# Kernel tuning notes

Hardware: AMD Instinct MI355X
Metric: run time of the kernel (lower is better)

The kernel has to match this reference:

```python
import jax, jax.numpy as jnp
import numpy as np

# Nemotron-H Mamba2 mixer decoder layer (prefill path, zero initial states,
# full context lengths). Dims per init_kwargs.
B, S, H = 1, 256, 4096
NH, P, G, N, K = 128, 64, 8, 128, 4   # num_heads, head_dim, n_groups, ssm_state_size, conv_kernel
D_INNER = NH * P                      # 8192
D_STATE = G * N                       # 1024
CONV_DIM = D_INNER + 2 * D_STATE      # 10240
IN_OUT = D_INNER + CONV_DIM + NH      # 18560
EPS = 1e-6


def setup_inputs() -> dict:
    key = jax.random.key(0)
    ks = jax.random.split(key, 8)
    sc = 0.02
    return {
        "hidden_states": jax.random.normal(ks[0], (B, S, H), jnp.float32),
        "conv_state": jnp.zeros((B, CONV_DIM, K - 1), jnp.float32),
        "ssm_state": jnp.zeros((B, NH, P, N), jnp.float32),
        "norm_weight": jnp.ones((H,), jnp.float32),
        "w_in": jax.random.normal(ks[1], (IN_OUT, H), jnp.float32) * sc,
        "conv_w": jax.random.normal(ks[2], (CONV_DIM, K), jnp.float32) * 0.2,
        "conv_b": jnp.zeros((CONV_DIM,), jnp.float32),
        "A_log": jax.random.uniform(ks[3], (NH,), jnp.float32, 0.0, 1.0),
        "D_param": jax.random.normal(ks[4], (NH,), jnp.float32) * 0.1,
        "dt_bias": jax.random.normal(ks[5], (NH,), jnp.float32) * 0.1,
        "ssm_norm_weight": jnp.ones((D_INNER,), jnp.float32),
        "w_out": jax.random.normal(ks[6], (H, D_INNER), jnp.float32) * sc,
    }


def _rmsnorm(x, w, eps=EPS):
    var = jnp.mean(x * x, axis=-1, keepdims=True)
    return x * jax.lax.rsqrt(var + eps) * w


def reference(hidden_states, conv_state, ssm_state, norm_weight, w_in, conv_w,
              conv_b, A_log, D_param, dt_bias, ssm_norm_weight, w_out):
    resid = hidden_states
    h = _rmsnorm(hidden_states, norm_weight)           # pre-mixer RMSNorm
    proj = jnp.einsum('bsh,oh->bso', h, w_in)          # in_proj [B,S,18560]
    gate = proj[..., :D_INNER]
    xconv = proj[..., D_INNER:D_INNER + CONV_DIM]
    dt = proj[..., D_INNER + CONV_DIM:]                # [B,S,NH]

    # depthwise causal conv1d, initial left context = conv_state
    xc = jnp.swapaxes(xconv, 1, 2)                     # [B,CONV_DIM,S]
    xpad = jnp.concatenate([conv_state, xc], axis=-1)  # [B,CONV_DIM,S+K-1]
    conv_state_out = xpad[:, :, -(K - 1):]
    y = conv_b[None, :, None]
    for j in range(K):                                 # K=4 taps, unrolled
        y = y + conv_w[:, j][None, :, None] * xpad[:, :, j:j + S]
    y = jax.nn.silu(jnp.swapaxes(y, 1, 2))             # [B,S,CONV_DIM]

    xs = y[..., :D_INNER].reshape(B, S, NH, P)
    Bs = y[..., D_INNER:D_INNER + D_STATE].reshape(B, S, G, N)
    Cs = y[..., D_INNER + D_STATE:].reshape(B, S, G, N)

    A = -jnp.exp(A_log)                                # [NH]
    dtp = jax.nn.softplus(dt + dt_bias)                # [B,S,NH]
    rep = NH // G
    Bh = jnp.repeat(Bs, rep, axis=2)                   # [B,S,NH,N]
    Ch = jnp.repeat(Cs, rep, axis=2)

    def step(state, inp):
        x_t, b_t, c_t, dt_t = inp                      # [B,NH,P],[B,NH,N],[B,NH,N],[B,NH]
        dA = jnp.exp(dt_t * A)                         # [B,NH]
        state = state * dA[..., None, None] + (dt_t[..., None] * x_t)[..., None] * b_t[:, :, None, :]
        y_t = jnp.einsum('bhpn,bhn->bhp', state, c_t)
        return state, y_t

    inps = (jnp.swapaxes(xs, 0, 1), jnp.swapaxes(Bh, 0, 1),
            jnp.swapaxes(Ch, 0, 1), jnp.swapaxes(dtp, 0, 1))
    ssm_state_out, ys = jax.lax.scan(step, ssm_state, inps)
    ys = jnp.swapaxes(ys, 0, 1) + D_param[None, None, :, None] * xs
    ssm_out = ys.reshape(B, S, D_INNER)

    # gated grouped RMSNorm (group_size = D_INNER // G = 1024)
    gated = ssm_out * jax.nn.silu(gate)
    gsize = D_INNER // G
    gg = gated.reshape(B, S, D_INNER // gsize, gsize)
    var = jnp.mean(gg * gg, axis=-1, keepdims=True)
    normed = (gg * jax.lax.rsqrt(var + EPS)).reshape(B, S, D_INNER) * ssm_norm_weight

    out = jnp.einsum('bsd,hd->bsh', normed, w_out)     # out_proj
    return resid + out, conv_state_out, ssm_state_out
```

## Files before the change

kernel.cpp:

```cpp
#include <hip/hip_runtime.h>
#include <hip/hip_bf16.h>

#define Sq 256
#define Hd 4096
#define NH 128
#define Pd 64
#define Gg 8
#define Nn 128
#define D_INNER 8192
#define D_STATE 1024
#define CONV_DIM 10240
#define IN_OUT 18560
#define DT_COL0 18432
#define EPSI 1e-6f

typedef _Float16 f16x8 __attribute__((ext_vector_type(8)));
typedef _Float16 f16x2 __attribute__((ext_vector_type(2)));
typedef float f32x4 __attribute__((ext_vector_type(4)));

__device__ inline ushort f2h(float f) {
  _Float16 h = (_Float16)f;
  return __builtin_bit_cast(ushort, h);
}
__device__ inline float h2f(ushort u) {
  return (float)__builtin_bit_cast(_Float16, u);
}
__device__ inline ushort f2h_lo(float f, ushort hi) {
  float hf = (float)__builtin_bit_cast(_Float16, hi);
  _Float16 l = (_Float16)(f - hf);
  return __builtin_bit_cast(ushort, l);
}
__device__ inline f16x2 pkrtz(float a, float b) {
  return __builtin_bit_cast(f16x2, __builtin_amdgcn_cvt_pkrtz(a, b));
}

__global__ __launch_bounds__(256) void rmsnorm_k(const float* __restrict__ x,
                                                 const float* __restrict__ w,
                                                 ushort* __restrict__ h_hi,
                                                 ushort* __restrict__ h_lo) {
  int s = blockIdx.x, t = threadIdx.x;
  const float4* row = reinterpret_cast<const float4*>(x + (size_t)s * Hd);
  const float4* wv  = reinterpret_cast<const float4*>(w);
  float4 v[4];
  float ss = 0.f;
#pragma unroll
  for (int i = 0; i < 4; i++) {
    v[i] = row[t + i * 256];
    ss += v[i].x * v[i].x + v[i].y * v[i].y + v[i].z * v[i].z + v[i].w * v[i].w;
  }
#pragma unroll
  for (int off = 32; off > 0; off >>= 1) ss += __shfl_xor(ss, off);
  __shared__ float red[4];
  if ((t & 63) == 0) red[t >> 6] = ss;
  __syncthreads();
  ss = red[0] + red[1] + red[2] + red[3];
  float scale = rsqrtf(ss * (1.f / (float)Hd) + EPSI);
  ushort4* hh = reinterpret_cast<ushort4*>(h_hi + (size_t)s * Hd);
  ushort4* hl = reinterpret_cast<ushort4*>(h_lo + (size_t)s * Hd);
#pragma unroll
  for (int i = 0; i < 4; i++) {
    float4 wi = wv[t + i * 256];
    float f0 = v[i].x * scale * wi.x, f1 = v[i].y * scale * wi.y;
    float f2 = v[i].z * scale * wi.z, f3 = v[i].w * scale * wi.w;
    ushort4 oh, ol;
    oh.x = f2h(f0); ol.x = f2h_lo(f0, oh.x);
    oh.y = f2h(f1); ol.y = f2h_lo(f1, oh.y);
    oh.z = f2h(f2); ol.z = f2h_lo(f2, oh.z);
    oh.w = f2h(f3); ol.w = f2h_lo(f3, oh.w);
    hh[t + i * 256] = oh;
    hl[t + i * 256] = ol;
  }
}

__global__ __launch_bounds__(256) void gemm_t128(const ushort* __restrict__ A,
                                                 const float* __restrict__ B,
                                                 float* __restrict__ C0,
                                                 ushort* __restrict__ Cp,
                                                 int ldc, int K, int kLen) {
  __shared__ __align__(16) ushort As[2][128 * 32];
  __shared__ __align__(16) ushort Bs[2][128 * 32];
  int t = threadIdx.x;
  int wave = t >> 6, lane = t & 63;
  int wr = wave >> 1, wc = wave & 1;
  int frow = lane & 15, gq = lane >> 4;
  int coltile = blockIdx.x >> 1;
  int rowBase = (blockIdx.x & 1) * 128;
  int bcol = coltile * 128;
  int z = blockIdx.z;
  int kStart = z * kLen;

  int ar = t >> 2;
  int ax = (ar >> 1) & 3;
  const ushort* ApG0 = A + (size_t)(rowBase + ar) * K + kStart + ((t & 3) ^ ax) * 8;
  const ushort* ApG1 = ApG0 + (size_t)64 * K;
  char* dstA0 = (char*)&As[0][0] + wave * 1024;
  char* dstA1 = (char*)&As[0][0] + 4096 + wave * 1024;

  int brow = t >> 1, bhalf = t & 1;
  int bx = (brow >> 1) & 3;
  const float* BpG = B + (size_t)(bcol + brow) * K + kStart + bhalf * 16;
  int bslot0 = ((2 * bhalf) ^ bx) * 16;
  int bslot1 = ((2 * bhalf + 1) ^ bx) * 16;
  float4 rb[4];

  f32x4 acc[4][4] = {};
  const int NT = kLen / 32;

#define ISSUE_B(kk) { _Pragma("unroll") for (int j = 0; j < 4; ++j) \
                        rb[j] = *(const float4*)(BpG + (kk) + j * 4); }
#define DMA_A(p, kk) { \
    __builtin_amdgcn_global_load_lds( \
        (const __attribute__((address_space(1))) void*)(ApG0 + (kk)), \
        (__attribute__((address_space(3))) void*)(dstA0 + (p) * 8192), 16, 0, 0); \
    __builtin_amdgcn_global_load_lds( \
        (const __attribute__((address_space(1))) void*)(ApG1 + (kk)), \
        (__attribute__((address_space(3))) void*)(dstA1 + (p) * 8192), 16, 0, 0); }
#define WRITE_B(p) { \
    union { f16x2 h2[8]; uint4 q[2]; } u; \
    u.h2[0] = pkrtz(rb[0].x, rb[0].y); u.h2[1] = pkrtz(rb[0].z, rb[0].w); \
    u.h2[2] = pkrtz(rb[1].x, rb[1].y); u.h2[3] = pkrtz(rb[1].z, rb[1].w); \
    u.h2[4] = pkrtz(rb[2].x, rb[2].y); u.h2[5] = pkrtz(rb[2].z, rb[2].w); \
    u.h2[6] = pkrtz(rb[3].x, rb[3].y); u.h2[7] = pkrtz(rb[3].z, rb[3].w); \
    char* bb = (char*)&Bs[0][0] + (p) * 8192 + brow * 64; \
    *(uint4*)(bb + bslot0) = u.q[0]; \
    *(uint4*)(bb + bslot1) = u.q[1]; }

  ISSUE_B(0)
  DMA_A(0, 0)
  WRITE_B(0)
  __syncthreads();

  for (int i = 0; i < NT; ++i) {
    int cur = i & 1;
    if (i + 1 < NT) {
      ISSUE_B((i + 1) * 32)
      DMA_A(cur ^ 1, (i + 1) * 32)
    }
    f16x8 af[4], bf[4];
#pragma unroll
    for (int m = 0; m < 4; ++m) {
      int row = wr * 64 + m * 16 + frow;
      af[m] = *(const f16x8*)((const char*)&As[0][0] + cur * 8192 + row * 64 +
                              ((gq ^ ((row >> 1) & 3)) * 16));
    }
#pragma unroll
    for (int n = 0; n < 4; ++n) {
      int row = wc * 64 + n * 16 + frow;
      bf[n] = *(const f16x8*)((const char*)&Bs[0][0] + cur * 8192 + row * 64 +
                              ((gq ^ ((row >> 1) & 3)) * 16));
    }
#pragma unroll
    for (int m = 0; m < 4; ++m)
#pragma unroll
      for (int n = 0; n < 4; ++n)
        acc[m][n] = __builtin_amdgcn_mfma_f32_16x16x32_f16(af[m], bf[n], acc[m][n], 0, 0, 0);
    __builtin_amdgcn_sched_barrier(0);
    if (i + 1 < NT) WRITE_B(cur ^ 1)
    __syncthreads();
  }
#undef ISSUE_B
#undef DMA_A
#undef WRITE_B

  if (z == 0) {
#pragma unroll
    for (int m = 0; m < 4; ++m) {
      int row0 = rowBase + wr * 64 + m * 16 + (lane >> 4) * 4;
#pragma unroll
      for (int n = 0; n < 4; ++n) {
        int col = bcol + wc * 64 + n * 16 + frow;
#pragma unroll
        for (int r = 0; r < 4; ++r)
          C0[(size_t)(row0 + r) * ldc + col] = acc[m][n][r];
      }
    }
  } else {
    ushort* Cz = Cp + (size_t)(z - 1) * Sq * ldc;
#pragma unroll
    for (int m = 0; m < 4; ++m) {
      int row0 = rowBase + wr * 64 + m * 16 + (lane >> 4) * 4;
#pragma unroll
      for (int n = 0; n < 4; ++n) {
        int col = bcol + wc * 64 + n * 16 + frow;
#pragma unroll
        for (int r = 0; r < 4; ++r)
          Cz[(size_t)(row0 + r) * ldc + col] = f2h(acc[m][n][r]);
      }
    }
  }
}

template<int BN, bool SPLIT>
__global__ __launch_bounds__(256) void gemm_mfma(const ushort* __restrict__ A_hi,
                                                 const ushort* __restrict__ A_lo,
                                                 const float* __restrict__ B,
                                                 float* __restrict__ C,
                                                 int ldc, int K, int kLen,
                                                 int bcol0, int M) {
  constexpr int BK = 64;
  constexpr int LDA = 72;
  constexpr int N_REP = BN / 32;
  constexpr int BQN = (BN == 128) ? 8 : 4;
  __shared__ __align__(16) ushort As[64 * LDA];
  __shared__ __align__(16) ushort Bs[BN * LDA];
  __shared__ __align__(16) ushort AsL[SPLIT ? 64 * LDA : 1];
  __shared__ __align__(16) ushort BsL[SPLIT ? BN * LDA : 1];

  int t = threadIdx.x;
  int wave = t >> 6, lane = t & 63;
  int wr = wave >> 1, wc = wave & 1;
  int frow = lane & 15, fk = (lane >> 4) * 8;
  int rowBase = blockIdx.x * 64;
  int bcol = bcol0 + blockIdx.y * BN;
  int ccol = blockIdx.y * BN;
  int kStart = blockIdx.z * kLen;
  C += (size_t)blockIdx.z * M * ldc;

  int arow = t >> 2, ak = (t & 3) * 16;
  const ushort* Ap  = A_hi + (size_t)(rowBase + arow) * K + ak;
  const ushort* ApL = SPLIT ? (A_lo + (size_t)(rowBase + arow) * K + ak) : nullptr;

  int brow, bq;
  if constexpr (BN == 128) { brow = t >> 1; bq = (t & 1) * 32; }
  else                     { brow = t >> 2; bq = (t & 3) * 16; }
  const float* Bp = B + (size_t)(bcol + brow) * K + bq;

  f32x4 acc[2][N_REP] = {};
  uint4 aPre[2], aPreL[2];
  float4 bPre[BQN];

  auto loadK = [&](int kk) {
    aPre[0] = *reinterpret_cast<const uint4*>(Ap + kk);
    aPre[1] = *reinterpret_cast<const uint4*>(Ap + kk + 8);
    if constexpr (SPLIT) {
      aPreL[0] = *reinterpret_cast<const uint4*>(ApL + kk);
      aPreL[1] = *reinterpret_cast<const uint4*>(ApL + kk + 8);
    }
#pragma unroll
    for (int j = 0; j < BQN; ++j)
      bPre[j] = *reinterpret_cast<const float4*>(Bp + kk + j * 4);
  };

  loadK(kStart);
  for (int ki = 0; ki < kLen; ki += BK) {
    __syncthreads();
    *reinterpret_cast<uint4*>(&As[arow * LDA + ak])     = aPre[0];
    *reinterpret_cast<uint4*>(&As[arow * LDA + ak + 8]) = aPre[1];
    if constexpr (SPLIT) {
      *reinterpret_cast<uint4*>(&AsL[arow * LDA + ak])     = aPreL[0];
      *reinterpret_cast<uint4*>(&AsL[arow * LDA + ak + 8]) = aPreL[1];
    }
    {
      ushort hb[BQN * 4];
      ushort lb[SPLIT ? BQN * 4 : 1];
      const float* bf = reinterpret_cast<const float*>(bPre);
#pragma unroll
      for (int j = 0; j < BQN * 4; ++j) {
        hb[j] = f2h(bf[j]);
        if constexpr (SPLIT) lb[j] = f2h_lo(bf[j], hb[j]);
      }
#pragma unroll
      for (int j = 0; j < BQN / 2; ++j)
        *reinterpret_cast<uint4*>(&Bs[brow * LDA + bq + j * 8]) =
            reinterpret_cast<const uint4*>(hb)[j];
      if constexpr (SPLIT) {
#pragma unroll
        for (int j = 0; j < BQN / 2; ++j)
          *reinterpret_cast<uint4*>(&BsL[brow * LDA + bq + j * 8]) =
              reinterpret_cast<const uint4*>(lb)[j];
      }
    }
    __syncthreads();
    if (ki + BK < kLen) loadK(kStart + ki + BK);
    f16x8 af[2][2], bfv[N_REP][2];
    f16x8 afL[SPLIT ? 2 : 1][2], bfL[SPLIT ? N_REP : 1][2];
#pragma unroll
    for (int m = 0; m < 2; ++m)
#pragma unroll
      for (int kh = 0; kh < 2; ++kh) {
        af[m][kh] = *reinterpret_cast<const f16x8*>(
            &As[(wr * 32 + m * 16 + frow) * LDA + kh * 32 + fk]);
        if constexpr (SPLIT)
          afL[m][kh] = *reinterpret_cast<const f16x8*>(
              &AsL[(wr * 32 + m * 16 + frow) * LDA + kh * 32 + fk]);
      }
#pragma unroll
    for (int n = 0; n < N_REP; ++n)
#pragma unroll
      for (int kh = 0; kh < 2; ++kh) {
        bfv[n][kh] = *reinterpret_cast<const f16x8*>(
            &Bs[(wc * (BN / 2) + n * 16 + frow) * LDA + kh * 32 + fk]);
        if constexpr (SPLIT)
          bfL[n][kh] = *reinterpret_cast<const f16x8*>(
              &BsL[(wc * (BN / 2) + n * 16 + frow) * LDA + kh * 32 + fk]);
      }
#pragma unroll
    for (int kh = 0; kh < 2; ++kh)
#pragma unroll
      for (int m = 0; m < 2; ++m)
#pragma unroll
        for (int n = 0; n < N_REP; ++n) {
          acc[m][n] = __builtin_amdgcn_mfma_f32_16x16x32_f16(af[m][kh], bfv[n][kh], acc[m][n], 0, 0, 0);
          if constexpr (SPLIT) {
            acc[m][n] = __builtin_amdgcn_mfma_f32_16x16x32_f16(af[m][kh], bfL[n][kh], acc[m][n], 0, 0, 0);
            acc[m][n] = __builtin_amdgcn_mfma_f32_16x16x32_f16(afL[m][kh], bfv[n][kh], acc[m][n], 0, 0, 0);
          }
        }
  }

#pragma unroll
  for (int m = 0; m < 2; ++m) {
    int row0 = rowBase + wr * 32 + m * 16 + (lane >> 4) * 4;
#pragma unroll
    for (int n = 0; n < N_REP; ++n) {
      int col = ccol + wc * (BN / 2) + n * 16 + frow;
#pragma unroll
      for (int r = 0; r < 4; ++r)
        C[(size_t)(row0 + r) * ldc + col] = acc[m][n][r];
    }
  }
}

__global__ __launch_bounds__(256) void reduce_in_k(float* __restrict__ proj,
                                                   const ushort* __restrict__ pp) {
  int i = blockIdx.x * 256 + threadIdx.x;
  const size_t PL = (size_t)Sq * IN_OUT;
  float4 o = reinterpret_cast<const float4*>(proj)[i];
#pragma unroll
  for (int zz = 0; zz < 3; ++zz) {
    ushort4 hv = reinterpret_cast<const ushort4*>(pp + zz * PL)[i];
    o.x += h2f(hv.x); o.y += h2f(hv.y); o.z += h2f(hv.z); o.w += h2f(hv.w);
  }
  reinterpret_cast<float4*>(proj)[i] = o;
}

__global__ __launch_bounds__(256) void conv_silu_k(const float* __restrict__ proj,
                                                   const float* __restrict__ cstate,
                                                   const float* __restrict__ cw,
                                                   const float* __restrict__ cb,
                                                   float* __restrict__ y,
                                                   float* __restrict__ out1) {
  int s = blockIdx.y;
  if (s == Sq) {
    int c = blockIdx.x * 256 + threadIdx.x;
#pragma unroll
    for (int tt = 0; tt < 3; ++tt)
      out1[c * 3 + tt] = proj[(size_t)(Sq - 3 + tt) * IN_OUT + D_INNER + c];
    return;
  }
  int c = blockIdx.x * 256 + threadIdx.x;
  float acc = cb[c];
  float4 w4 = *reinterpret_cast<const float4*>(cw + c * 4);
  float wj[4] = {w4.x, w4.y, w4.z, w4.w};
#pragma unroll
  for (int j = 0; j < 4; j++) {
    int si = s + j - 3;
    float v = (si < 0) ? cstate[c * 3 + (si + 3)]
                       : proj[(size_t)si * IN_OUT + D_INNER + c];
    acc += wj[j] * v;
  }
  float sig = 1.f / (1.f + expf(-acc));
  y[(size_t)s * CONV_DIM + c] = acc * sig;
}

#define CS 16
__global__ __launch_bounds__(256) void ssm_scan_k(const float* __restrict__ y_conv,
                                                  const float* __restrict__ dtfix,
                                                  const float* __restrict__ dt_bias,
                                                  const float* __restrict__ sstate_in,
                                                  const float* __restrict__ A_log,
                                                  const float* __restrict__ D_param,
                                                  float* __restrict__ ys_out,
                                                  float* __restrict__ sstate_out) {
  int h = blockIdx.x >> 2;
  int pb = (blockIdx.x & 3) * 16;
  int t = threadIdx.x;
  int ng = t & 15, pl = t >> 4;
  int g = h >> 4;
  float A = -expf(A_log[h]);
  float Dp = D_param[h];
  float bias = dt_bias[h];

  float st[8];
  {
    const float* sp = sstate_in + ((size_t)h * Pd + pb + pl) * Nn + ng * 8;
    float4 v = *reinterpret_cast<const float4*>(sp);
    float4 w = *reinterpret_cast<const float4*>(sp + 4);
    st[0] = v.x; st[1] = v.y; st[2] = v.z; st[3] = v.w;
    st[4] = w.x; st[5] = w.y; st[6] = w.z; st[7] = w.w;
  }

  __shared__ __align__(16) float ybuf[CS][272];
  __shared__ float dts[CS];
  int lr = t >> 4;
  int lc = t & 15;

  for (int ch = 0; ch < Sq / CS; ++ch) {
    int s0 = ch * CS;
    __syncthreads();
    const float* rowp = y_conv + (size_t)(s0 + lr) * CONV_DIM;
#pragma unroll
    for (int j = 0; j < 5; ++j) {
      int c = lc + 16 * j;
      if (c < 68) {
        const float* src;
        int off;
        if (c < 4)       { src = rowp + h * 64 + pb;                      off = c * 4; }
        else if (c < 36) { src = rowp + D_INNER + g * 128;                off = (c - 4) * 4; }
        else             { src = rowp + D_INNER + D_STATE + g * 128;      off = (c - 36) * 4; }
        int dst = (c < 4) ? c * 4 : (c < 36 ? 16 + (c - 4) * 4 : 144 + (c - 36) * 4);
        *reinterpret_cast<float4*>(&ybuf[lr][dst]) = *reinterpret_cast<const float4*>(src + off);
      }
    }
    if (t < CS) {
      float v = bias;
      int idx = (s0 + t) * NH + h;
#pragma unroll
      for (int zz = 0; zz < 32; ++zz) v += dtfix[zz * (Sq * NH) + idx];
      dts[t] = (v > 20.f) ? v : log1pf(expf(v));
    }
    __syncthreads();

#pragma unroll 4
    for (int stp = 0; stp < CS; ++stp) {
      float dt = dts[stp];
      float dA = expf(dt * A);
      float x0 = ybuf[stp][pl];
      float dtx = dt * x0;
      float4 b0 = *reinterpret_cast<const float4*>(&ybuf[stp][16 + ng * 8]);
      float4 b1 = *reinterpret_cast<const float4*>(&ybuf[stp][16 + ng * 8 + 4]);
      float4 c0 = *reinterpret_cast<const float4*>(&ybuf[stp][144 + ng * 8]);
      float4 c1 = *reinterpret_cast<const float4*>(&ybuf[stp][144 + ng * 8 + 4]);
      float y0;
      st[0] = st[0] * dA + dtx * b0.x;  y0  = st[0] * c0.x;
      st[1] = st[1] * dA + dtx * b0.y;  y0 += st[1] * c0.y;
      st[2] = st[2] * dA + dtx * b0.z;  y0 += st[2] * c0.z;
      st[3] = st[3] * dA + dtx * b0.w;  y0 += st[3] * c0.w;
      st[4] = st[4] * dA + dtx * b1.x;  y0 += st[4] * c1.x;
      st[5] = st[5] * dA + dtx * b1.y;  y0 += st[5] * c1.y;
      st[6] = st[6] * dA + dtx * b1.z;  y0 += st[6] * c1.z;
      st[7] = st[7] * dA + dtx * b1.w;  y0 += st[7] * c1.w;
      y0 += __shfl_xor(y0, 1); y0 += __shfl_xor(y0, 2);
      y0 += __shfl_xor(y0, 4); y0 += __shfl_xor(y0, 8);
      if (ng == 0)
        ys_out[(size_t)(s0 + stp) * D_INNER + h * 64 + pb + pl] = y0 + Dp * x0;
    }
  }

  float* so = sstate_out + ((size_t)h * Pd + pb + pl) * Nn + ng * 8;
  *reinterpret_cast<float4*>(so)     = make_float4(st[0], st[1], st[2], st[3]);
  *reinterpret_cast<float4*>(so + 4) = make_float4(st[4], st[5], st[6], st[7]);
}

__global__ __launch_bounds__(256) void gated_norm_k(const float* __restrict__ ys,
                                                    const float* __restrict__ proj,
                                                    const float* __restrict__ w,
                                                    ushort* __restrict__ out_h) {
  int s = blockIdx.x, g = blockIdx.y, t = threadIdx.x;
  float vals[4];
  float ss = 0.f;
#pragma unroll
  for (int i = 0; i < 4; i++) {
    int d = g * 1024 + i * 256 + t;
    float gate = proj[(size_t)s * IN_OUT + d];
    float v = ys[(size_t)s * D_INNER + d] * (gate / (1.f + expf(-gate)));
    vals[i] = v;
    ss += v * v;
  }
#pragma unroll
  for (int off = 32; off > 0; off >>= 1) ss += __shfl_xor(ss, off);
  __shared__ float red[4];
  if ((t & 63) == 0) red[t >> 6] = ss;
  __syncthreads();
  ss = red[0] + red[1] + red[2] + red[3];
  float scale = rsqrtf(ss * (1.f / 1024.f) + EPSI);
#pragma unroll
  for (int i = 0; i < 4; i++) {
    int d = g * 1024 + i * 256 + t;
    out_h[(size_t)s * D_INNER + d] = f2h(vals[i] * scale * w[d]);
  }
}

__global__ __launch_bounds__(256) void reduce_out_k(const float* __restrict__ p0,
                                                    const ushort* __restrict__ pph,
                                                    const float* __restrict__ hidden,
                                                    float* __restrict__ out0) {
  int i = blockIdx.x * 256 + threadIdx.x;
  const size_t PL = (size_t)Sq * Hd;
  float4 o = reinterpret_cast<const float4*>(hidden)[i];
  float4 a = reinterpret_cast<const float4*>(p0)[i];
  o.x += a.x; o.y += a.y; o.z += a.z; o.w += a.w;
#pragma unroll
  for (int zz = 0; zz < 15; ++zz) {
    ushort4 hv = reinterpret_cast<const ushort4*>(pph + zz * PL)[i];
    o.x += h2f(hv.x); o.y += h2f(hv.y); o.z += h2f(hv.z); o.w += h2f(hv.w);
  }
  reinterpret_cast<float4*>(out0)[i] = o;
}

extern "C" void kernel_launch(void* const* d_in, const int* in_sizes, int n_in,
                              void* d_out, int out_size, void* d_ws, size_t ws_size,
                              hipStream_t stream) {
  const float* hidden    = (const float*)d_in[0];
  const float* cstate_in = (const float*)d_in[1];
  const float* sstate_in = (const float*)d_in[2];
  const float* norm_w    = (const float*)d_in[3];
  const float* w_in      = (const float*)d_in[4];
  const float* conv_w    = (const float*)d_in[5];
  const float* conv_b    = (const float*)d_in[6];
  const float* A_log     = (const float*)d_in[7];
  const float* D_param   = (const float*)d_in[8];
  const float* dt_bias   = (const float*)d_in[9];
  const float* ssm_nw    = (const float*)d_in[10];
  const float* w_out     = (const float*)d_in[11];

  float* out0 = (float*)d_out;
  float* out1 = out0 + (size_t)Sq * Hd;
  float* out2 = out1 + (size_t)CONV_DIM * 3;

  ushort* h_hi  = (ushort*)d_ws;
  ushort* h_lo  = h_hi + (size_t)Sq * Hd;
  float*  proj  = (float*)(h_lo + (size_t)Sq * Hd);
  ushort* pp_in = (ushort*)(proj + (size_t)Sq * IN_OUT);
  float*  y_conv = (float*)pp_in;
  float*  dtp   = y_conv + (size_t)Sq * CONV_DIM;
  float*  ys    = dtp + (size_t)Sq * NH;
  ushort* ys_h  = (ushort*)(ys + (size_t)Sq * D_INNER);
  float*  dtfix = (float*)(ys_h + (size_t)Sq * D_INNER);
  float*  op0    = (float*)d_ws;
  ushort* pp_out = (ushort*)(op0 + (size_t)Sq * Hd);

  rmsnorm_k<<<Sq, 256, 0, stream>>>(hidden, norm_w, h_hi, h_lo);
  gemm_t128<<<dim3(2 * (IN_OUT / 128), 1, 4), 256, 0, stream>>>(
      h_hi, w_in, proj, pp_in, IN_OUT, Hd, Hd / 4);
  reduce_in_k<<<(Sq * IN_OUT / 4) / 256, 256, 0, stream>>>(proj, pp_in);
  gemm_mfma<64, true><<<dim3(4, 2, 32), 256, 0, stream>>>(
      h_hi, h_lo, w_in, dtfix, NH, Hd, Hd / 32, DT_COL0, Sq);
  conv_silu_k<<<dim3(CONV_DIM / 256, Sq + 1), 256, 0, stream>>>(
      proj, cstate_in, conv_w, conv_b, y_conv, out1);
  ssm_scan_k<<<NH * 4, 256, 0, stream>>>(y_conv, dtfix, dt_bias, sstate_in,
                                         A_log, D_param, ys, out2);
  gated_norm_k<<<dim3(Sq, Gg), 256, 0, stream>>>(ys, proj, ssm_nw, ys_h);
  gemm_t128<<<dim3(2 * (Hd / 128), 1, 16), 256, 0, stream>>>(
      ys_h, w_out, op0, pp_out, Hd, D_INNER, D_INNER / 16);
  reduce_out_k<<<(Sq * Hd / 4) / 256, 256, 0, stream>>>(op0, pp_out, hidden, out0);
}
```

Before: 349.0 us.

## Widen GEMM tile to full 256 rows with 512-thread blocks sharing B

The GEMM kernel now covers all 256 sequence rows in one block of 8 waves instead of splitting rows across two 128-row blocks. Each block converts and stages the fp32 weight tile to fp16 once rather than twice, which halves global weight reads and conversion work. In exchange the grid has half as many blocks, each block uses more LDS, and fewer blocks fit on a CU, so latency hiding may suffer on the smaller out_proj grid.

```diff
diff --git a/kernel.cpp b/kernel.cpp
--- a/kernel.cpp
+++ b/kernel.cpp
@@ -72,58 +72,51 @@
   }
 }
 
-__global__ __launch_bounds__(256) void gemm_t128(const ushort* __restrict__ A,
+__global__ __launch_bounds__(512) void gemm_w256(const ushort* __restrict__ A,
                                                  const float* __restrict__ B,
                                                  float* __restrict__ C0,
                                                  ushort* __restrict__ Cp,
                                                  int ldc, int K, int kLen) {
-  __shared__ __align__(16) ushort As[2][128 * 32];
+  __shared__ __align__(16) ushort As[2][256 * 32];
   __shared__ __align__(16) ushort Bs[2][128 * 32];
   int t = threadIdx.x;
   int wave = t >> 6, lane = t & 63;
   int wr = wave >> 1, wc = wave & 1;
   int frow = lane & 15, gq = lane >> 4;
-  int coltile = blockIdx.x >> 1;
-  int rowBase = (blockIdx.x & 1) * 128;
-  int bcol = coltile * 128;
+  int bcol = blockIdx.x * 128;
   int z = blockIdx.z;
   int kStart = z * kLen;
 
   int ar = t >> 2;
   int ax = (ar >> 1) & 3;
-  const ushort* ApG0 = A + (size_t)(rowBase + ar) * K + kStart + ((t & 3) ^ ax) * 8;
-  const ushort* ApG1 = ApG0 + (size_t)64 * K;
+  const ushort* ApG0 = A + (size_t)ar * K + kStart + ((t & 3) ^ ax) * 8;
+  const ushort* ApG1 = ApG0 + (size_t)128 * K;
   char* dstA0 = (char*)&As[0][0] + wave * 1024;
-  char* dstA1 = (char*)&As[0][0] + 4096 + wave * 1024;
-
-  int brow = t >> 1, bhalf = t & 1;
+  char* dstA1 = (char*)&As[0][0] + 8192 + wave * 1024;
+
+  int brow = t >> 2, bq4 = t & 3;
   int bx = (brow >> 1) & 3;
-  const float* BpG = B + (size_t)(bcol + brow) * K + kStart + bhalf * 16;
-  int bslot0 = ((2 * bhalf) ^ bx) * 16;
-  int bslot1 = ((2 * bhalf + 1) ^ bx) * 16;
-  float4 rb[4];
+  const float* BpG = B + (size_t)(bcol + brow) * K + kStart + bq4 * 8;
+  int bslot = ((bq4) ^ bx) * 16;
+  float4 rb[2];
 
   f32x4 acc[4][4] = {};
   const int NT = kLen / 32;
 
-#define ISSUE_B(kk) { _Pragma("unroll") for (int j = 0; j < 4; ++j) \
-                        rb[j] = *(const float4*)(BpG + (kk) + j * 4); }
+#define ISSUE_B(kk) { rb[0] = *(const float4*)(BpG + (kk)); \
+                      rb[1] = *(const float4*)(BpG + (kk) + 4); }
 #define DMA_A(p, kk) { \
     __builtin_amdgcn_global_load_lds( \
         (const __attribute__((address_space(1))) void*)(ApG0 + (kk)), \
-        (__attribute__((address_space(3))) void*)(dstA0 + (p) * 8192), 16, 0, 0); \
+        (__attribute__((address_space(3))) void*)(dstA0 + (p) * 16384), 16, 0, 0); \
     __builtin_amdgcn_global_load_lds( \
         (const __attribute__((address_space(1))) void*)(ApG1 + (kk)), \
-        (__attribute__((address_space(3))) void*)(dstA1 + (p) * 8192), 16, 0, 0); }
+        (__attribute__((address_space(3))) void*)(dstA1 + (p) * 16384), 16, 0, 0); }
 #define WRITE_B(p) { \
-    union { f16x2 h2[8]; uint4 q[2]; } u; \
+    union { f16x2 h2[4]; uint4 q; } u; \
     u.h2[0] = pkrtz(rb[0].x, rb[0].y); u.h2[1] = pkrtz(rb[0].z, rb[0].w); \
     u.h2[2] = pkrtz(rb[1].x, rb[1].y); u.h2[3] = pkrtz(rb[1].z, rb[1].w); \
-    u.h2[4] = pkrtz(rb[2].x, rb[2].y); u.h2[5] = pkrtz(rb[2].z, rb[2].w); \
-    u.h2[6] = pkrtz(rb[3].x, rb[3].y); u.h2[7] = pkrtz(rb[3].z, rb[3].w); \
-    char* bb = (char*)&Bs[0][0] + (p) * 8192 + brow * 64; \
-    *(uint4*)(bb + bslot0) = u.q[0]; \
-    *(uint4*)(bb + bslot1) = u.q[1]; }
+    *(uint4*)((char*)&Bs[0][0] + (p) * 8192 + brow * 64 + bslot) = u.q; }
 
   ISSUE_B(0)
   DMA_A(0, 0)
@@ -140,7 +133,7 @@
 #pragma unroll
     for (int m = 0; m < 4; ++m) {
       int row = wr * 64 + m * 16 + frow;
-      af[m] = *(const f16x8*)((const char*)&As[0][0] + cur * 8192 + row * 64 +
+      af[m] = *(const f16x8*)((const char*)&As[0][0] + cur * 16384 + row * 64 +
                               ((gq ^ ((row >> 1) & 3)) * 16));
     }
 #pragma unroll
@@ -165,7 +158,7 @@
   if (z == 0) {
 #pragma unroll
     for (int m = 0; m < 4; ++m) {
-      int row0 = rowBase + wr * 64 + m * 16 + (lane >> 4) * 4;
+      int row0 = wr * 64 + m * 16 + (lane >> 4) * 4;
 #pragma unroll
       for (int n = 0; n < 4; ++n) {
         int col = bcol + wc * 64 + n * 16 + frow;
@@ -178,7 +171,7 @@
     ushort* Cz = Cp + (size_t)(z - 1) * Sq * ldc;
 #pragma unroll
     for (int m = 0; m < 4; ++m) {
-      int row0 = rowBase + wr * 64 + m * 16 + (lane >> 4) * 4;
+      int row0 = wr * 64 + m * 16 + (lane >> 4) * 4;
 #pragma unroll
       for (int n = 0; n < 4; ++n) {
         int col = bcol + wc * 64 + n * 16 + frow;
@@ -531,7 +524,7 @@
   ushort* pp_out = (ushort*)(op0 + (size_t)Sq * Hd);
 
   rmsnorm_k<<<Sq, 256, 0, stream>>>(hidden, norm_w, h_hi, h_lo);
-  gemm_t128<<<dim3(2 * (IN_OUT / 128), 1, 4), 256, 0, stream>>>(
+  gemm_w256<<<dim3(IN_OUT / 128, 1, 4), 512, 0, stream>>>(
       h_hi, w_in, proj, pp_in, IN_OUT, Hd, Hd / 4);
   reduce_in_k<<<(Sq * IN_OUT / 4) / 256, 256, 0, stream>>>(proj, pp_in);
   gemm_mfma<64, true><<<dim3(4, 2, 32), 256, 0, stream>>>(
@@ -541,7 +534,7 @@
   ssm_scan_k<<<NH * 4, 256, 0, stream>>>(y_conv, dtfix, dt_bias, sstate_in,
                                          A_log, D_param, ys, out2);
   gated_norm_k<<<dim3(Sq, Gg), 256, 0, stream>>>(ys, proj, ssm_nw, ys_h);
-  gemm_t128<<<dim3(2 * (Hd / 128), 1, 16), 256, 0, stream>>>(
+  gemm_w256<<<dim3(Hd / 128, 1, 16), 512, 0, stream>>>(
       ys_h, w_out, op0, pp_out, Hd, D_INNER, D_INNER / 16);
   reduce_out_k<<<(Sq * Hd / 4) / 256, 256, 0, stream>>>(op0, pp_out, hidden, out0);
 }
```

New measurement: 345.6 us. Within noise of the previous version (-1.0%).
